# Optimization experiments

Measured on AMD Instinct MI355X. Metric: run time of the kernel, lower is better.

The kernel has to match this reference:

```python
import jax, jax.numpy as jnp
import numpy as np

RADIUS = 0.4
K = 32
EPS = 1e-5


def ball_query(xyz, new_xyz, radius, k):
    """xyz: (B,N,3), new_xyz: (B,M,3) -> idx (B,M,k) int32.
    Replicates CUDA ball_query: first k points within radius (in index order),
    padded with the first found index."""
    N = xyz.shape[1]
    # squared distances (B,M,N)
    d2 = jnp.sum((new_xyz[:, :, None, :] - xyz[:, None, :, :]) ** 2, axis=-1)
    within = d2 < radius * radius
    order = jnp.arange(N, dtype=jnp.int32)
    key = jnp.where(within, order[None, None, :], N)
    idx_sorted = jnp.argsort(key, axis=-1)[..., :k].astype(jnp.int32)  # (B,M,k)
    cnt = within.sum(axis=-1)  # (B,M)
    first = idx_sorted[..., :1]
    slot = jnp.arange(k)[None, None, :]
    return jnp.where(slot < cnt[..., None], idx_sorted, first)


def gather_bmk(x_bnc, idx):
    """x_bnc: (B,N,C), idx: (B,M,K) -> (B,M,K,C)"""
    return jnp.take_along_axis(x_bnc[:, None, :, :], idx[..., None], axis=2)


def conv_bn_relu(x, w, b, gamma, beta):
    """x: (B,Cin,M,K); w: (Cout,Cin). 1x1 Conv2d + BatchNorm2d (train stats) + ReLU."""
    x = jnp.einsum('bcmk,oc->bomk', x, w) + b[None, :, None, None]
    mu = x.mean(axis=(0, 2, 3), keepdims=True)
    var = x.var(axis=(0, 2, 3), keepdims=True)
    x = gamma[None, :, None, None] * (x - mu) * jax.lax.rsqrt(var + EPS) + beta[None, :, None, None]
    return jax.nn.relu(x)


def setup_inputs() -> dict:
    key = jax.random.key(0)
    ks = jax.random.split(key, 16)
    B, N, C, M = 4, 16384, 128, 1024
    mlp = [131, 128, 128, 256]
    inp = {
        'points_xyz': jax.random.normal(ks[0], (B, N, 3), dtype=jnp.float32),
        'features': jax.random.normal(ks[1], (B, C, N), dtype=jnp.float32),
        'indices': jax.random.randint(ks[2], (B, M), 0, N, dtype=jnp.int32),
    }
    for i in range(3):
        cin, cout = mlp[i], mlp[i + 1]
        inp[f'w{i+1}'] = jax.random.normal(ks[3 + 4 * i], (cout, cin), dtype=jnp.float32) / np.sqrt(cin)
        inp[f'b{i+1}'] = jnp.zeros((cout,), dtype=jnp.float32)
        inp[f'g{i+1}'] = jnp.ones((cout,), dtype=jnp.float32)
        inp[f'beta{i+1}'] = jnp.zeros((cout,), dtype=jnp.float32)
    return inp


def reference(points_xyz, features, indices,
              w1, b1, g1, beta1, w2, b2, g2, beta2, w3, b3, g3, beta3):
    # sample centers: new_xyz (B,M,3)
    new_xyz = jnp.take_along_axis(points_xyz, indices[..., None], axis=1)
    # ball query + group
    idx = ball_query(points_xyz, new_xyz, RADIUS, K)            # (B,M,K)
    grouped_xyz = gather_bmk(points_xyz, idx) - new_xyz[:, :, None, :]  # (B,M,K,3)
    grouped_feat = gather_bmk(features.transpose(0, 2, 1), idx)         # (B,M,K,C)
    x = jnp.concatenate([grouped_xyz, grouped_feat], axis=-1)           # (B,M,K,3+C)
    x = x.transpose(0, 3, 1, 2)                                         # (B,3+C,M,K)
    # shared MLP (1x1 Conv2d + BN + ReLU)
    x = conv_bn_relu(x, w1, b1, g1, beta1)
    x = conv_bn_relu(x, w2, b2, g2, beta2)
    x = conv_bn_relu(x, w3, b3, g3, beta3)
    # max pool over K -> (B, Cout, M)
    new_features = x.max(axis=-1)
    return new_xyz, new_features
```

## Files before the change

### kernel.cpp

```cpp
#include <hip/hip_runtime.h>

#define B_ 4
#define N_ 16384
#define C_ 128
#define M_ 1024
#define K_ 32
#define NTOT (B_*M_*K_)
#define RAD2 0.16f
#define EPS_ 1e-5f

typedef unsigned short ushort_t;
typedef __bf16 bf16x8 __attribute__((ext_vector_type(8)));
typedef float f32x4 __attribute__((ext_vector_type(4)));

__device__ __forceinline__ float b2f(ushort_t u){
  unsigned int x = ((unsigned int)u) << 16;
  return __builtin_bit_cast(float, x);
}
__device__ __forceinline__ ushort_t f2b(float f){
  return __builtin_bit_cast(ushort_t, (__bf16)f);
}

__global__ __launch_bounds__(256) void prep_all_k(
    const float* __restrict__ feat, ushort_t* __restrict__ ftr_t,
    const float* __restrict__ xyz, const int* __restrict__ indices,
    float* __restrict__ new_xyz, int* __restrict__ idx,
    const float* __restrict__ w1, const float* __restrict__ w2, const float* __restrict__ w3,
    ushort_t* __restrict__ W1b, ushort_t* __restrict__ W2b, ushort_t* __restrict__ W3b,
    float* __restrict__ stats)
{
  __shared__ float T[32][133];
  int bid = blockIdx.x;
  int t = threadIdx.x;

  if (bid < 1024){
    int wv = t >> 6, lane = t & 63;
    int g = bid*4 + wv;
    int b = g >> 10;
    const float* pb = xyz + (size_t)b*N_*3;
    const float4* pb4 = (const float4*)pb;
    int qi = indices[g];
    float qx = pb[qi*3+0], qy = pb[qi*3+1], qz = pb[qi*3+2];
    if (lane < 3) new_xyz[g*3 + lane] = pb[qi*3 + lane];

    int cnt = 0, firstIdx = 0;
    int* op = idx + g*K_;

    float4 buf0[6], buf1[6];
    #pragma unroll
    for (int i = 0; i < 6; i++) buf0[i] = pb4[lane*6 + i];

    unsigned long long below = (lane == 0) ? 0ull : ((~0ull) >> (64 - lane));

    auto process = [&](const float4* buf, int chunk){
      const float* f = (const float*)buf;
      unsigned int local_mask = 0;
      #pragma unroll
      for (int j = 0; j < 8; j++){
        float dx = f[j*3+0]-qx, dy = f[j*3+1]-qy, dz = f[j*3+2]-qz;
        if (dx*dx + dy*dy + dz*dz < RAD2) local_mask |= (1u << j);
      }
      unsigned long long many = __ballot(local_mask != 0);
      if (many == 0ull) return;
      int base = chunk*512;
      unsigned long long mj[8];
      #pragma unroll
      for (int j = 0; j < 8; j++) mj[j] = __ballot((local_mask >> j) & 1u);
      int excl = 0, total = 0;
      #pragma unroll
      for (int j = 0; j < 8; j++){
        excl  += __popcll(mj[j] & below);
        total += __popcll(mj[j]);
      }
      if (cnt == 0){
        int l0 = __builtin_ctzll(many);
        int j0 = 0;
        #pragma unroll
        for (int j = 7; j >= 0; j--) if ((mj[j] >> l0) & 1ull) j0 = j;
        firstIdx = base + l0*8 + j0;
      }
      int sl = cnt + excl;
      unsigned int m = local_mask;
      while (m && sl < K_){
        int j = __builtin_ctz(m); m &= m - 1u;
        op[sl++] = base + lane*8 + j;
      }
      cnt += total;
    };

    for (int chunk = 0; chunk < 32; chunk += 2){
      if (chunk + 1 < 32){
        #pragma unroll
        for (int i = 0; i < 6; i++) buf1[i] = pb4[(chunk+1)*384 + lane*6 + i];
      }
      process(buf0, chunk);
      if (cnt >= K_) break;
      if (chunk + 2 < 32){
        #pragma unroll
        for (int i = 0; i < 6; i++) buf0[i] = pb4[(chunk+2)*384 + lane*6 + i];
      }
      process(buf1, chunk + 1);
      if (cnt >= K_) break;
    }
    if (cnt < K_){
      for (int s = cnt + lane; s < K_; s += 64) op[s] = firstIdx;
    }
  } else if (bid < 3072){
    int bb = bid - 1024;
    int b = bb >> 9, ntile = bb & 511;
    int n0 = ntile * 32;
    int nl = t & 31;
    #pragma unroll
    for (int ci = 0; ci < 16; ci++){
      int c = ci*8 + (t >> 5);
      T[nl][c] = feat[((size_t)b*C_ + c)*N_ + n0 + nl];
    }
    __syncthreads();
    #pragma unroll
    for (int ii = 0; ii < 2; ii++){
      int v = ii*256 + t;
      int n2 = v >> 4, seg = v & 15;
      union { ushort_t u[8]; uint4 q; } pk;
      #pragma unroll
      for (int j = 0; j < 8; j++) pk.u[j] = f2b(T[n2][seg*8 + j]);
      *(uint4*)(ftr_t + ((size_t)b*N_ + n0 + n2)*C_ + seg*8) = pk.q;
    }
  } else {
    const int T1 = 128*160, T2 = 128*128;
    int e = (bid - 3072)*256 + t;
    if (e < T1){
      int o = e / 160, c = e % 160;
      float v = 0.f;
      if (c < 128) v = w1[o*131 + 3 + c];
      else if (c < 131) v = w1[o*131 + (c - 128)];
      W1b[e] = f2b(v);
    } else if (e < T1+T2){
      int e2 = e - T1;
      W2b[e2] = f2b(w2[e2]);
    } else {
      int e3 = e - T1 - T2;
      W3b[e3] = f2b(w3[e3]);
    }
    if (bid == 3072){
      #pragma unroll
      for (int j = 0; j < 6; j++) stats[j*256 + t] = 0.f;
    }
  }
}

__global__ __launch_bounds__(256, 4) void conv1_k(
    const float* __restrict__ xyz, const ushort_t* __restrict__ ftr_t,
    const int* __restrict__ idx, const float* __restrict__ new_xyz,
    const ushort_t* __restrict__ W1b, const float* __restrict__ b1,
    ushort_t* __restrict__ Y1, float* __restrict__ sumO, float* __restrict__ sqO)
{
  __shared__ alignas(16) ushort_t Xs[2][32*168];
  __shared__ alignas(16) float Ys[2][32*68];
  int t = threadIdx.x;
  int wv = t >> 6, lane = t & 63, quad = lane >> 4, l15 = lane & 15;
  int row = t >> 3, chunk = t & 7;
  int col0 = (blockIdx.x & 1) * 64;
  int blk = blockIdx.x >> 1;

  if (t < 128){
    int rr = t >> 2, cc = t & 3;
    *(uint4*)(Xs[0] + rr*168 + 128 + cc*8) = make_uint4(0,0,0,0);
    *(uint4*)(Xs[1] + rr*168 + 128 + cc*8) = make_uint4(0,0,0,0);
  }
  bf16x8 wf[5];
  #pragma unroll
  for (int kt = 0; kt < 5; kt++)
    wf[kt] = *(const bf16x8*)(W1b + (col0 + wv*16 + l15)*160 + kt*32 + quad*8);
  float bs_r = b1[col0 + wv*16 + l15];
  float s = 0.f, s2 = 0.f;

  const int GPB = 8;
  int g0 = blk * GPB;
  int b = g0 >> 10;
  int ia[GPB], ibv[GPB];
  #pragma unroll
  for (int i = 0; i < GPB; i++){
    ia[i]  = idx[(g0+i)*K_ + row];
    ibv[i] = idx[(g0+i)*K_ + (t & 31)];
  }
  uint4 r0, r1;
  float p3x, p3y, p3z, q3x, q3y, q3z;
  {
    const ushort_t* src = ftr_t + ((size_t)b*N_ + ia[0])*C_ + chunk*16;
    r0 = *(const uint4*)src; r1 = *(const uint4*)(src + 8);
    if (t < 32){
      const float* pp = xyz + ((size_t)b*N_ + ibv[0])*3;
      const float* qq = new_xyz + (size_t)g0*3;
      p3x = pp[0]; p3y = pp[1]; p3z = pp[2];
      q3x = qq[0]; q3y = qq[1]; q3z = qq[2];
    }
  }
  for (int i = 0; i < GPB; i++){
    int p = i & 1;
    ushort_t* X = Xs[p];
    *(uint4*)(X + row*168 + chunk*16) = r0;
    *(uint4*)(X + row*168 + chunk*16 + 8) = r1;
    if (t < 32){
      unsigned int u0 = (unsigned int)f2b(p3x-q3x) | ((unsigned int)f2b(p3y-q3y) << 16);
      unsigned int u1 = (unsigned int)f2b(p3z-q3z);
      *(uint2*)(X + t*168 + 128) = make_uint2(u0, u1);
    }
    if (i + 1 < GPB){
      const ushort_t* src = ftr_t + ((size_t)b*N_ + ia[i+1])*C_ + chunk*16;
      r0 = *(const uint4*)src; r1 = *(const uint4*)(src + 8);
      if (t < 32){
        const float* pp = xyz + ((size_t)b*N_ + ibv[i+1])*3;
        const float* qq = new_xyz + (size_t)(g0+i+1)*3;
        p3x = pp[0]; p3y = pp[1]; p3z = pp[2];
        q3x = qq[0]; q3y = qq[1]; q3z = qq[2];
      }
    }
    __syncthreads();
    bf16x8 af[2][5];
    #pragma unroll
    for (int mt = 0; mt < 2; mt++)
      #pragma unroll
      for (int kt = 0; kt < 5; kt++)
        af[mt][kt] = *(const bf16x8*)(X + (mt*16 + l15)*168 + kt*32 + quad*8);
    f32x4 acc[2] = {(f32x4){0,0,0,0}, (f32x4){0,0,0,0}};
    #pragma unroll
    for (int kt = 0; kt < 5; kt++){
      acc[0] = __builtin_amdgcn_mfma_f32_16x16x32_bf16(af[0][kt], wf[kt], acc[0], 0,0,0);
      acc[1] = __builtin_amdgcn_mfma_f32_16x16x32_bf16(af[1][kt], wf[kt], acc[1], 0,0,0);
    }
    {
      int o = wv*16 + l15;
      float* Yw = Ys[p];
      #pragma unroll
      for (int mt = 0; mt < 2; mt++)
        #pragma unroll
        for (int r = 0; r < 4; r++){
          float v = acc[mt][r] + bs_r;
          s += v; s2 += v*v;
          Yw[(mt*16 + quad*4 + r)*68 + o] = v;
        }
    }
    if (i > 0){
      const float* yp = &Ys[p^1][row*68 + chunk*8];
      f32x4 y0 = *(const f32x4*)(yp);
      f32x4 y1 = *(const f32x4*)(yp + 4);
      union { ushort_t u[8]; uint4 q; } p0;
      #pragma unroll
      for (int j = 0; j < 4; j++){
        p0.u[j] = f2b(y0[j]); p0.u[4+j] = f2b(y1[j]);
      }
      *(uint4*)(Y1 + ((size_t)(g0+i-1)*K_ + row)*128 + col0 + chunk*8) = p0.q;
    }
  }
  __syncthreads();
  {
    const float* yp = &Ys[(GPB-1)&1][row*68 + chunk*8];
    f32x4 y0 = *(const f32x4*)(yp);
    f32x4 y1 = *(const f32x4*)(yp + 4);
    union { ushort_t u[8]; uint4 q; } p0;
    #pragma unroll
    for (int j = 0; j < 4; j++){
      p0.u[j] = f2b(y0[j]); p0.u[4+j] = f2b(y1[j]);
    }
    *(uint4*)(Y1 + ((size_t)(g0+GPB-1)*K_ + row)*128 + col0 + chunk*8) = p0.q;
  }
  s  += __shfl_xor(s, 16);  s  += __shfl_xor(s, 32);
  s2 += __shfl_xor(s2, 16); s2 += __shfl_xor(s2, 32);
  if (quad == 0){
    int o = col0 + wv*16 + l15;
    atomicAdd(&sumO[o], s);
    atomicAdd(&sqO[o], s2);
  }
}

template<int COUT, bool MAXMIN, int MINB>
__global__ __launch_bounds__(256, MINB) void convB_k(
    const ushort_t* __restrict__ Yin, const ushort_t* __restrict__ Wb,
    const float* __restrict__ bias, const float* __restrict__ g_bn,
    const float* __restrict__ beta_bn, const float* __restrict__ sumI,
    const float* __restrict__ sqI, ushort_t* __restrict__ Yout,
    unsigned int* __restrict__ Ymm, float* __restrict__ sumO, float* __restrict__ sqO)
{
  constexpr int HALF = COUT/2;
  constexpr int NT = HALF/64;
  __shared__ alignas(16) ushort_t Xs[2][32*136];
  __shared__ alignas(16) float Ys[MAXMIN ? 1 : 2][MAXMIN ? 4 : 32*68];
  int t = threadIdx.x;
  int wv = t >> 6, lane = t & 63, quad = lane >> 4, l15 = lane & 15;
  int row = t >> 3, chunk = t & 7;
  int col0 = (blockIdx.x & 1) * HALF;
  int blk = blockIdx.x >> 1;

  float a_r[16], d_r[16];
  #pragma unroll
  for (int j = 0; j < 16; j++){
    int c = chunk*16 + j;
    float mu  = sumI[c] * (1.f/NTOT);
    float var = sqI[c]  * (1.f/NTOT) - mu*mu;
    float a = g_bn[c] * rsqrtf(var + EPS_);
    a_r[j] = a; d_r[j] = beta_bn[c] - a*mu;
  }
  bf16x8 wf[NT][4];
  #pragma unroll
  for (int nt = 0; nt < NT; nt++)
    #pragma unroll
    for (int kt = 0; kt < 4; kt++)
      wf[nt][kt] = *(const bf16x8*)(Wb + (col0 + wv*(NT*16) + nt*16 + l15)*128 + kt*32 + quad*8);
  float bs_r[NT];
  #pragma unroll
  for (int nt = 0; nt < NT; nt++) bs_r[nt] = bias[col0 + wv*(NT*16) + nt*16 + l15];
  float s[NT], s2[NT];
  #pragma unroll
  for (int nt = 0; nt < NT; nt++){ s[nt] = 0.f; s2[nt] = 0.f; }

  const int GPB = 8;
  int g0 = blk * GPB;
  uint4 r0, r1;
  {
    const ushort_t* src = Yin + ((size_t)g0*K_ + row)*128 + chunk*16;
    r0 = *(const uint4*)src; r1 = *(const uint4*)(src + 8);
  }
  for (int i = 0; i < GPB; i++){
    int p = i & 1;
    int g = g0 + i;
    ushort_t* X = Xs[p];
    union { ushort_t u[8]; uint4 q; } i0, i1, o0, o1;
    i0.q = r0; i1.q = r1;
    #pragma unroll
    for (int j = 0; j < 8; j++){
      o0.u[j] = f2b(fmaxf(a_r[j]  *b2f(i0.u[j]) + d_r[j],   0.f));
      o1.u[j] = f2b(fmaxf(a_r[8+j]*b2f(i1.u[j]) + d_r[8+j], 0.f));
    }
    *(uint4*)(X + row*136 + chunk*16) = o0.q;
    *(uint4*)(X + row*136 + chunk*16 + 8) = o1.q;
    if (i + 1 < GPB){
      const ushort_t* src = Yin + ((size_t)(g+1)*K_ + row)*128 + chunk*16;
      r0 = *(const uint4*)src; r1 = *(const uint4*)(src + 8);
    }
    __syncthreads();
    f32x4 acc[NT][2];
    #pragma unroll
    for (int nt = 0; nt < NT; nt++){ acc[nt][0] = (f32x4){0,0,0,0}; acc[nt][1] = (f32x4){0,0,0,0}; }
    #pragma unroll
    for (int kt = 0; kt < 4; kt++){
      bf16x8 A0 = *(const bf16x8*)(X + (l15)*136      + kt*32 + quad*8);
      bf16x8 A1 = *(const bf16x8*)(X + (16 + l15)*136 + kt*32 + quad*8);
      #pragma unroll
      for (int nt = 0; nt < NT; nt++){
        acc[nt][0] = __builtin_amdgcn_mfma_f32_16x16x32_bf16(A0, wf[nt][kt], acc[nt][0], 0,0,0);
        acc[nt][1] = __builtin_amdgcn_mfma_f32_16x16x32_bf16(A1, wf[nt][kt], acc[nt][1], 0,0,0);
      }
    }
    if constexpr (!MAXMIN){
      {
        int o = wv*16 + l15;
        float* Yw = Ys[p];
        #pragma unroll
        for (int mt = 0; mt < 2; mt++)
          #pragma unroll
          for (int r = 0; r < 4; r++){
            float v = acc[0][mt][r] + bs_r[0];
            s[0] += v; s2[0] += v*v;
            Yw[(mt*16 + quad*4 + r)*68 + o] = v;
          }
      }
      if (i > 0){
        const float* yp = &Ys[p^1][row*68 + chunk*8];
        f32x4 y0 = *(const f32x4*)(yp);
        f32x4 y1 = *(const f32x4*)(yp + 4);
        union { ushort_t u[8]; uint4 q; } p0;
        #pragma unroll
        for (int j = 0; j < 4; j++){
          p0.u[j] = f2b(y0[j]); p0.u[4+j] = f2b(y1[j]);
        }
        *(uint4*)(Yout + ((size_t)(g-1)*K_ + row)*128 + col0 + chunk*8) = p0.q;
      }
    } else {
      #pragma unroll
      for (int nt = 0; nt < NT; nt++){
        float v0 = acc[nt][0][0] + bs_r[nt];
        float mx = v0, mn = v0;
        s[nt] += v0; s2[nt] += v0*v0;
        #pragma unroll
        for (int mt = 0; mt < 2; mt++)
          #pragma unroll
          for (int r = 0; r < 4; r++){
            if (mt == 0 && r == 0) continue;
            float v = acc[nt][mt][r] + bs_r[nt];
            s[nt] += v; s2[nt] += v*v;
            mx = fmaxf(mx, v); mn = fminf(mn, v);
          }
        mx = fmaxf(mx, __shfl_xor(mx, 16)); mx = fmaxf(mx, __shfl_xor(mx, 32));
        mn = fminf(mn, __shfl_xor(mn, 16)); mn = fminf(mn, __shfl_xor(mn, 32));
        if (quad == 0){
          int o = col0 + wv*(NT*16) + nt*16 + l15;
          Ymm[(size_t)g*256 + o] = (unsigned int)f2b(mx) | ((unsigned int)f2b(mn) << 16);
        }
      }
    }
  }
  if constexpr (!MAXMIN){
    __syncthreads();
    const float* yp = &Ys[(GPB-1)&1][row*68 + chunk*8];
    f32x4 y0 = *(const f32x4*)(yp);
    f32x4 y1 = *(const f32x4*)(yp + 4);
    union { ushort_t u[8]; uint4 q; } p0;
    #pragma unroll
    for (int j = 0; j < 4; j++){
      p0.u[j] = f2b(y0[j]); p0.u[4+j] = f2b(y1[j]);
    }
    *(uint4*)(Yout + ((size_t)(g0+GPB-1)*K_ + row)*128 + col0 + chunk*8) = p0.q;
  }
  #pragma unroll
  for (int nt = 0; nt < NT; nt++){
    s[nt]  += __shfl_xor(s[nt], 16);  s[nt]  += __shfl_xor(s[nt], 32);
    s2[nt] += __shfl_xor(s2[nt], 16); s2[nt] += __shfl_xor(s2[nt], 32);
    if (quad == 0){
      int o = col0 + wv*(NT*16) + nt*16 + l15;
      atomicAdd(&sumO[o], s[nt]);
      atomicAdd(&sqO[o], s2[nt]);
    }
  }
}

__global__ __launch_bounds__(256) void finalize_k(
    const unsigned int* __restrict__ Ymm, const float* __restrict__ g3,
    const float* __restrict__ beta3, const float* __restrict__ sum3,
    const float* __restrict__ sq3, float* __restrict__ out)
{
  __shared__ float T[16][264];
  __shared__ float abn[256], dbn[256];
  int t = threadIdx.x;
  int b = blockIdx.x >> 6;
  int m0 = (blockIdx.x & 63) * 16;
  {
    float mu  = sum3[t] * (1.f/NTOT);
    float var = sq3[t]  * (1.f/NTOT) - mu*mu;
    float a = g3[t] * rsqrtf(var + EPS_);
    abn[t] = a; dbn[t] = beta3[t] - a*mu;
  }
  __syncthreads();
  #pragma unroll
  for (int i = 0; i < 4; i++){
    int v4 = i*256 + t;
    int m = v4 >> 6, oq = (v4 & 63) * 4;
    uint4 w = *(const uint4*)(Ymm + ((size_t)(b*M_ + m0 + m))*256 + oq);
    unsigned int wsv[4] = {w.x, w.y, w.z, w.w};
    float r[4];
    #pragma unroll
    for (int j = 0; j < 4; j++){
      int o = oq + j;
      float mx = b2f((ushort_t)(wsv[j] & 0xffffu));
      float mn = b2f((ushort_t)(wsv[j] >> 16));
      float a = abn[o];
      float val = (a >= 0.f) ? (a*mx + dbn[o]) : (a*mn + dbn[o]);
      r[j] = fmaxf(val, 0.f);
    }
    *(f32x4*)(&T[m][oq]) = *(f32x4*)r;
  }
  __syncthreads();
  #pragma unroll
  for (int p = 0; p < 4; p++){
    int o = p*64 + (t >> 2), c = t & 3;
    float4 v = make_float4(T[c*4+0][o], T[c*4+1][o], T[c*4+2][o], T[c*4+3][o]);
    *(float4*)(out + ((size_t)(b*256 + o))*M_ + m0 + c*4) = v;
  }
}

extern "C" void kernel_launch(void* const* d_in, const int* in_sizes, int n_in,
                              void* d_out, int out_size, void* d_ws, size_t ws_size,
                              hipStream_t stream)
{
  (void)in_sizes; (void)n_in; (void)out_size; (void)ws_size;
  const float* xyz  = (const float*)d_in[0];
  const float* feat = (const float*)d_in[1];
  const int*   inds = (const int*)d_in[2];
  const float* w1 = (const float*)d_in[3];
  const float* b1 = (const float*)d_in[4];
  const float* g1 = (const float*)d_in[5];
  const float* be1= (const float*)d_in[6];
  const float* w2 = (const float*)d_in[7];
  const float* b2 = (const float*)d_in[8];
  const float* g2 = (const float*)d_in[9];
  const float* be2= (const float*)d_in[10];
  const float* w3 = (const float*)d_in[11];
  const float* b3 = (const float*)d_in[12];
  const float* g3 = (const float*)d_in[13];
  const float* be3= (const float*)d_in[14];

  char* ws = (char*)d_ws;
  float* stats = (float*)ws;
  float* s1sum = stats + 0*256;  float* s1sq = stats + 1*256;
  float* s2sum = stats + 2*256;  float* s2sq = stats + 3*256;
  float* s3sum = stats + 4*256;  float* s3sq = stats + 5*256;
  size_t off = 6*256*sizeof(float);
  int* idx = (int*)(ws + off);                off += (size_t)B_*M_*K_*4;
  ushort_t* ftr_t = (ushort_t*)(ws + off);    off += (size_t)B_*N_*C_*2;
  ushort_t* W1b = (ushort_t*)(ws + off);      off += 128*160*2;
  ushort_t* W2b = (ushort_t*)(ws + off);      off += 128*128*2;
  ushort_t* W3b = (ushort_t*)(ws + off);      off += 256*128*2;
  ushort_t* Y1 = (ushort_t*)(ws + off);       off += (size_t)NTOT*128*2;
  ushort_t* Y2 = (ushort_t*)(ws + off);       off += (size_t)NTOT*128*2;
  unsigned int* Ymm = (unsigned int*)(ws + off); off += (size_t)B_*M_*256*4;

  float* new_xyz  = (float*)d_out;
  float* out_feat = (float*)d_out + (size_t)B_*M_*3;

  prep_all_k<<<3344, 256, 0, stream>>>(feat, ftr_t, xyz, inds, new_xyz, idx,
                                       w1, w2, w3, W1b, W2b, W3b, stats);
  conv1_k<<<1024, 256, 0, stream>>>(xyz, ftr_t, idx, new_xyz, W1b, b1, Y1, s1sum, s1sq);
  convB_k<128,false,4><<<1024, 256, 0, stream>>>(Y1, W2b, b2, g1, be1, s1sum, s1sq, Y2, nullptr, s2sum, s2sq);
  convB_k<256,true ,4><<<1024, 256, 0, stream>>>(Y2, W3b, b3, g2, be2, s2sum, s2sq, nullptr, Ymm, s3sum, s3sq);
  finalize_k<<<256, 256, 0, stream>>>(Ymm, g3, be3, s3sum, s3sq, out_feat);
}
```

Before: 209.4 us.

## Fuse ball query into conv1 kernel with pairwise inter-block spin barrier

Moves the ball-query work out of the prep kernel and into the first conv kernel. Each block computes the neighbour indices for 4 groups, then syncs with its partner block through a global atomic counter before both consume the 8 groups' indices. This shrinks the prep kernel and overlaps the ball query with conv1's per-block work, at the cost of a spin-wait that assumes both blocks in a pair are co-resident, which risks deadlock or stalls.

```diff
diff --git a/kernel.cpp b/kernel.cpp
--- a/kernel.cpp
+++ b/kernel.cpp
@@ -21,93 +21,18 @@
   return __builtin_bit_cast(ushort_t, (__bf16)f);
 }
 
-__global__ __launch_bounds__(256) void prep_all_k(
+__global__ __launch_bounds__(256) void prep2_k(
     const float* __restrict__ feat, ushort_t* __restrict__ ftr_t,
-    const float* __restrict__ xyz, const int* __restrict__ indices,
-    float* __restrict__ new_xyz, int* __restrict__ idx,
     const float* __restrict__ w1, const float* __restrict__ w2, const float* __restrict__ w3,
     ushort_t* __restrict__ W1b, ushort_t* __restrict__ W2b, ushort_t* __restrict__ W3b,
-    float* __restrict__ stats)
+    float* __restrict__ stats, unsigned int* __restrict__ pairbar)
 {
   __shared__ float T[32][133];
   int bid = blockIdx.x;
   int t = threadIdx.x;
 
-  if (bid < 1024){
-    int wv = t >> 6, lane = t & 63;
-    int g = bid*4 + wv;
-    int b = g >> 10;
-    const float* pb = xyz + (size_t)b*N_*3;
-    const float4* pb4 = (const float4*)pb;
-    int qi = indices[g];
-    float qx = pb[qi*3+0], qy = pb[qi*3+1], qz = pb[qi*3+2];
-    if (lane < 3) new_xyz[g*3 + lane] = pb[qi*3 + lane];
-
-    int cnt = 0, firstIdx = 0;
-    int* op = idx + g*K_;
-
-    float4 buf0[6], buf1[6];
-    #pragma unroll
-    for (int i = 0; i < 6; i++) buf0[i] = pb4[lane*6 + i];
-
-    unsigned long long below = (lane == 0) ? 0ull : ((~0ull) >> (64 - lane));
-
-    auto process = [&](const float4* buf, int chunk){
-      const float* f = (const float*)buf;
-      unsigned int local_mask = 0;
-      #pragma unroll
-      for (int j = 0; j < 8; j++){
-        float dx = f[j*3+0]-qx, dy = f[j*3+1]-qy, dz = f[j*3+2]-qz;
-        if (dx*dx + dy*dy + dz*dz < RAD2) local_mask |= (1u << j);
-      }
-      unsigned long long many = __ballot(local_mask != 0);
-      if (many == 0ull) return;
-      int base = chunk*512;
-      unsigned long long mj[8];
-      #pragma unroll
-      for (int j = 0; j < 8; j++) mj[j] = __ballot((local_mask >> j) & 1u);
-      int excl = 0, total = 0;
-      #pragma unroll
-      for (int j = 0; j < 8; j++){
-        excl  += __popcll(mj[j] & below);
-        total += __popcll(mj[j]);
-      }
-      if (cnt == 0){
-        int l0 = __builtin_ctzll(many);
-        int j0 = 0;
-        #pragma unroll
-        for (int j = 7; j >= 0; j--) if ((mj[j] >> l0) & 1ull) j0 = j;
-        firstIdx = base + l0*8 + j0;
-      }
-      int sl = cnt + excl;
-      unsigned int m = local_mask;
-      while (m && sl < K_){
-        int j = __builtin_ctz(m); m &= m - 1u;
-        op[sl++] = base + lane*8 + j;
-      }
-      cnt += total;
-    };
-
-    for (int chunk = 0; chunk < 32; chunk += 2){
-      if (chunk + 1 < 32){
-        #pragma unroll
-        for (int i = 0; i < 6; i++) buf1[i] = pb4[(chunk+1)*384 + lane*6 + i];
-      }
-      process(buf0, chunk);
-      if (cnt >= K_) break;
-      if (chunk + 2 < 32){
-        #pragma unroll
-        for (int i = 0; i < 6; i++) buf0[i] = pb4[(chunk+2)*384 + lane*6 + i];
-      }
-      process(buf1, chunk + 1);
-      if (cnt >= K_) break;
-    }
-    if (cnt < K_){
-      for (int s = cnt + lane; s < K_; s += 64) op[s] = firstIdx;
-    }
-  } else if (bid < 3072){
-    int bb = bid - 1024;
-    int b = bb >> 9, ntile = bb & 511;
+  if (bid < 2048){
+    int b = bid >> 9, ntile = bid & 511;
     int n0 = ntile * 32;
     int nl = t & 31;
     #pragma unroll
@@ -125,9 +50,9 @@
       for (int j = 0; j < 8; j++) pk.u[j] = f2b(T[n2][seg*8 + j]);
       *(uint4*)(ftr_t + ((size_t)b*N_ + n0 + n2)*C_ + seg*8) = pk.q;
     }
-  } else {
+  } else if (bid < 2320){
     const int T1 = 128*160, T2 = 128*128;
-    int e = (bid - 3072)*256 + t;
+    int e = (bid - 2048)*256 + t;
     if (e < T1){
       int o = e / 160, c = e % 160;
       float v = 0.f;
@@ -141,107 +66,209 @@
       int e3 = e - T1 - T2;
       W3b[e3] = f2b(w3[e3]);
     }
-    if (bid == 3072){
-      #pragma unroll
-      for (int j = 0; j < 6; j++) stats[j*256 + t] = 0.f;
-    }
-  }
-}
-
-__global__ __launch_bounds__(256, 4) void conv1_k(
-    const float* __restrict__ xyz, const ushort_t* __restrict__ ftr_t,
-    const int* __restrict__ idx, const float* __restrict__ new_xyz,
+  } else {
+    #pragma unroll
+    for (int j = 0; j < 6; j++) stats[j*256 + t] = 0.f;
+    #pragma unroll
+    for (int j = t; j < 512; j += 256) pairbar[j] = 0u;
+  }
+}
+
+__global__ __launch_bounds__(256, 4) void ballconv1_k(
+    const float* __restrict__ xyz, const int* __restrict__ indices,
+    float* new_xyz, int* idx,
+    const ushort_t* __restrict__ ftr_t,
     const ushort_t* __restrict__ W1b, const float* __restrict__ b1,
-    ushort_t* __restrict__ Y1, float* __restrict__ sumO, float* __restrict__ sqO)
+    ushort_t* __restrict__ Y1, float* __restrict__ sumO, float* __restrict__ sqO,
+    unsigned int* pairbar)
 {
   __shared__ alignas(16) ushort_t Xs[2][32*168];
   __shared__ alignas(16) float Ys[2][32*68];
   int t = threadIdx.x;
-  int wv = t >> 6, lane = t & 63, quad = lane >> 4, l15 = lane & 15;
-  int row = t >> 3, chunk = t & 7;
-  int col0 = (blockIdx.x & 1) * 64;
-  int blk = blockIdx.x >> 1;
-
-  if (t < 128){
-    int rr = t >> 2, cc = t & 3;
-    *(uint4*)(Xs[0] + rr*168 + 128 + cc*8) = make_uint4(0,0,0,0);
-    *(uint4*)(Xs[1] + rr*168 + 128 + cc*8) = make_uint4(0,0,0,0);
-  }
-  bf16x8 wf[5];
-  #pragma unroll
-  for (int kt = 0; kt < 5; kt++)
-    wf[kt] = *(const bf16x8*)(W1b + (col0 + wv*16 + l15)*160 + kt*32 + quad*8);
-  float bs_r = b1[col0 + wv*16 + l15];
-  float s = 0.f, s2 = 0.f;
-
-  const int GPB = 8;
-  int g0 = blk * GPB;
-  int b = g0 >> 10;
-  int ia[GPB], ibv[GPB];
-  #pragma unroll
-  for (int i = 0; i < GPB; i++){
-    ia[i]  = idx[(g0+i)*K_ + row];
-    ibv[i] = idx[(g0+i)*K_ + (t & 31)];
-  }
-  uint4 r0, r1;
-  float p3x, p3y, p3z, q3x, q3y, q3z;
+  int bid = blockIdx.x;
+
   {
-    const ushort_t* src = ftr_t + ((size_t)b*N_ + ia[0])*C_ + chunk*16;
-    r0 = *(const uint4*)src; r1 = *(const uint4*)(src + 8);
-    if (t < 32){
-      const float* pp = xyz + ((size_t)b*N_ + ibv[0])*3;
-      const float* qq = new_xyz + (size_t)g0*3;
-      p3x = pp[0]; p3y = pp[1]; p3z = pp[2];
-      q3x = qq[0]; q3y = qq[1]; q3z = qq[2];
-    }
-  }
-  for (int i = 0; i < GPB; i++){
-    int p = i & 1;
-    ushort_t* X = Xs[p];
-    *(uint4*)(X + row*168 + chunk*16) = r0;
-    *(uint4*)(X + row*168 + chunk*16 + 8) = r1;
-    if (t < 32){
-      unsigned int u0 = (unsigned int)f2b(p3x-q3x) | ((unsigned int)f2b(p3y-q3y) << 16);
-      unsigned int u1 = (unsigned int)f2b(p3z-q3z);
-      *(uint2*)(X + t*168 + 128) = make_uint2(u0, u1);
-    }
-    if (i + 1 < GPB){
-      const ushort_t* src = ftr_t + ((size_t)b*N_ + ia[i+1])*C_ + chunk*16;
+    int wv = t >> 6, lane = t & 63;
+    int g = bid*4 + wv;
+    int b = g >> 10;
+    const float* pb = xyz + (size_t)b*N_*3;
+    const float4* pb4 = (const float4*)pb;
+    int qi = indices[g];
+    float qx = pb[qi*3+0], qy = pb[qi*3+1], qz = pb[qi*3+2];
+    if (lane < 3) new_xyz[g*3 + lane] = pb[qi*3 + lane];
+
+    int cnt = 0, firstIdx = 0;
+    int* op = idx + g*K_;
+
+    float4 buf0[6], buf1[6];
+    #pragma unroll
+    for (int i = 0; i < 6; i++) buf0[i] = pb4[lane*6 + i];
+
+    unsigned long long below = (lane == 0) ? 0ull : ((~0ull) >> (64 - lane));
+
+    auto process = [&](const float4* buf, int chunk){
+      const float* f = (const float*)buf;
+      unsigned int local_mask = 0;
+      #pragma unroll
+      for (int j = 0; j < 8; j++){
+        float dx = f[j*3+0]-qx, dy = f[j*3+1]-qy, dz = f[j*3+2]-qz;
+        if (dx*dx + dy*dy + dz*dz < RAD2) local_mask |= (1u << j);
+      }
+      unsigned long long many = __ballot(local_mask != 0);
+      if (many == 0ull) return;
+      int base = chunk*512;
+      unsigned long long mj[8];
+      #pragma unroll
+      for (int j = 0; j < 8; j++) mj[j] = __ballot((local_mask >> j) & 1u);
+      int excl = 0, total = 0;
+      #pragma unroll
+      for (int j = 0; j < 8; j++){
+        excl  += __popcll(mj[j] & below);
+        total += __popcll(mj[j]);
+      }
+      if (cnt == 0){
+        int l0 = __builtin_ctzll(many);
+        int j0 = 0;
+        #pragma unroll
+        for (int j = 7; j >= 0; j--) if ((mj[j] >> l0) & 1ull) j0 = j;
+        firstIdx = base + l0*8 + j0;
+      }
+      int sl = cnt + excl;
+      unsigned int m = local_mask;
+      while (m && sl < K_){
+        int j = __builtin_ctz(m); m &= m - 1u;
+        op[sl++] = base + lane*8 + j;
+      }
+      cnt += total;
+    };
+
+    for (int chunk = 0; chunk < 32; chunk += 2){
+      if (chunk + 1 < 32){
+        #pragma unroll
+        for (int i = 0; i < 6; i++) buf1[i] = pb4[(chunk+1)*384 + lane*6 + i];
+      }
+      process(buf0, chunk);
+      if (cnt >= K_) break;
+      if (chunk + 2 < 32){
+        #pragma unroll
+        for (int i = 0; i < 6; i++) buf0[i] = pb4[(chunk+2)*384 + lane*6 + i];
+      }
+      process(buf1, chunk + 1);
+      if (cnt >= K_) break;
+    }
+    if (cnt < K_){
+      for (int s = cnt + lane; s < K_; s += 64) op[s] = firstIdx;
+    }
+  }
+
+  __syncthreads();
+  __threadfence();
+  if (t == 0){
+    __hip_atomic_fetch_add(&pairbar[bid >> 1], 1u, __ATOMIC_RELEASE, __HIP_MEMORY_SCOPE_AGENT);
+    while (__hip_atomic_load(&pairbar[bid >> 1], __ATOMIC_ACQUIRE, __HIP_MEMORY_SCOPE_AGENT) < 2u) {}
+  }
+  __syncthreads();
+  __threadfence();
+
+  {
+    int wv = t >> 6, lane = t & 63, quad = lane >> 4, l15 = lane & 15;
+    int row = t >> 3, chunk = t & 7;
+    int col0 = (bid & 1) * 64;
+    int blk = bid >> 1;
+
+    if (t < 128){
+      int rr = t >> 2, cc = t & 3;
+      *(uint4*)(Xs[0] + rr*168 + 128 + cc*8) = make_uint4(0,0,0,0);
+      *(uint4*)(Xs[1] + rr*168 + 128 + cc*8) = make_uint4(0,0,0,0);
+    }
+    bf16x8 wf[5];
+    #pragma unroll
+    for (int kt = 0; kt < 5; kt++)
+      wf[kt] = *(const bf16x8*)(W1b + (col0 + wv*16 + l15)*160 + kt*32 + quad*8);
+    float bs_r = b1[col0 + wv*16 + l15];
+    float s = 0.f, s2 = 0.f;
+
+    const int GPB = 8;
+    int g0 = blk * GPB;
+    int b = g0 >> 10;
+    int ia[GPB], ibv[GPB];
+    #pragma unroll
+    for (int i = 0; i < GPB; i++){
+      ia[i]  = idx[(g0+i)*K_ + row];
+      ibv[i] = idx[(g0+i)*K_ + (t & 31)];
+    }
+    uint4 r0, r1;
+    float p3x, p3y, p3z, q3x, q3y, q3z;
+    {
+      const ushort_t* src = ftr_t + ((size_t)b*N_ + ia[0])*C_ + chunk*16;
       r0 = *(const uint4*)src; r1 = *(const uint4*)(src + 8);
       if (t < 32){
-        const float* pp = xyz + ((size_t)b*N_ + ibv[i+1])*3;
-        const float* qq = new_xyz + (size_t)(g0+i+1)*3;
+        const float* pp = xyz + ((size_t)b*N_ + ibv[0])*3;
+        const float* qq = new_xyz + (size_t)g0*3;
         p3x = pp[0]; p3y = pp[1]; p3z = pp[2];
         q3x = qq[0]; q3y = qq[1]; q3z = qq[2];
       }
     }
+    for (int i = 0; i < GPB; i++){
+      int p = i & 1;
+      ushort_t* X = Xs[p];
+      *(uint4*)(X + row*168 + chunk*16) = r0;
+      *(uint4*)(X + row*168 + chunk*16 + 8) = r1;
+      if (t < 32){
+        unsigned int u0 = (unsigned int)f2b(p3x-q3x) | ((unsigned int)f2b(p3y-q3y) << 16);
+        unsigned int u1 = (unsigned int)f2b(p3z-q3z);
+        *(uint2*)(X + t*168 + 128) = make_uint2(u0, u1);
+      }
+      if (i + 1 < GPB){
+        const ushort_t* src = ftr_t + ((size_t)b*N_ + ia[i+1])*C_ + chunk*16;
+        r0 = *(const uint4*)src; r1 = *(const uint4*)(src + 8);
+        if (t < 32){
+          const float* pp = xyz + ((size_t)b*N_ + ibv[i+1])*3;
+          const float* qq = new_xyz + (size_t)(g0+i+1)*3;
+          p3x = pp[0]; p3y = pp[1]; p3z = pp[2];
+          q3x = qq[0]; q3y = qq[1]; q3z = qq[2];
+        }
+      }
+      __syncthreads();
+      bf16x8 af[2][5];
+      #pragma unroll
+      for (int mt = 0; mt < 2; mt++)
+        #pragma unroll
+        for (int kt = 0; kt < 5; kt++)
+          af[mt][kt] = *(const bf16x8*)(X + (mt*16 + l15)*168 + kt*32 + quad*8);
+      f32x4 acc[2] = {(f32x4){0,0,0,0}, (f32x4){0,0,0,0}};
+      #pragma unroll
+      for (int kt = 0; kt < 5; kt++){
+        acc[0] = __builtin_amdgcn_mfma_f32_16x16x32_bf16(af[0][kt], wf[kt], acc[0], 0,0,0);
+        acc[1] = __builtin_amdgcn_mfma_f32_16x16x32_bf16(af[1][kt], wf[kt], acc[1], 0,0,0);
+      }
+      {
+        int o = wv*16 + l15;
+        float* Yw = Ys[p];
+        #pragma unroll
+        for (int mt = 0; mt < 2; mt++)
+          #pragma unroll
+          for (int r = 0; r < 4; r++){
+            float v = acc[mt][r] + bs_r;
+            s += v; s2 += v*v;
+            Yw[(mt*16 + quad*4 + r)*68 + o] = v;
+          }
+      }
+      if (i > 0){
+        const float* yp = &Ys[p^1][row*68 + chunk*8];
+        f32x4 y0 = *(const f32x4*)(yp);
+        f32x4 y1 = *(const f32x4*)(yp + 4);
+        union { ushort_t u[8]; uint4 q; } p0;
+        #pragma unroll
+        for (int j = 0; j < 4; j++){
+          p0.u[j] = f2b(y0[j]); p0.u[4+j] = f2b(y1[j]);
+        }
+        *(uint4*)(Y1 + ((size_t)(g0+i-1)*K_ + row)*128 + col0 + chunk*8) = p0.q;
+      }
+    }
     __syncthreads();
-    bf16x8 af[2][5];
-    #pragma unroll
-    for (int mt = 0; mt < 2; mt++)
-      #pragma unroll
-      for (int kt = 0; kt < 5; kt++)
-        af[mt][kt] = *(const bf16x8*)(X + (mt*16 + l15)*168 + kt*32 + quad*8);
-    f32x4 acc[2] = {(f32x4){0,0,0,0}, (f32x4){0,0,0,0}};
-    #pragma unroll
-    for (int kt = 0; kt < 5; kt++){
-      acc[0] = __builtin_amdgcn_mfma_f32_16x16x32_bf16(af[0][kt], wf[kt], acc[0], 0,0,0);
-      acc[1] = __builtin_amdgcn_mfma_f32_16x16x32_bf16(af[1][kt], wf[kt], acc[1], 0,0,0);
-    }
     {
-      int o = wv*16 + l15;
-      float* Yw = Ys[p];
-      #pragma unroll
-      for (int mt = 0; mt < 2; mt++)
-        #pragma unroll
-        for (int r = 0; r < 4; r++){
-          float v = acc[mt][r] + bs_r;
-          s += v; s2 += v*v;
-          Yw[(mt*16 + quad*4 + r)*68 + o] = v;
-        }
-    }
-    if (i > 0){
-      const float* yp = &Ys[p^1][row*68 + chunk*8];
+      const float* yp = &Ys[(GPB-1)&1][row*68 + chunk*8];
       f32x4 y0 = *(const f32x4*)(yp);
       f32x4 y1 = *(const f32x4*)(yp + 4);
       union { ushort_t u[8]; uint4 q; } p0;
@@ -249,27 +276,15 @@
       for (int j = 0; j < 4; j++){
         p0.u[j] = f2b(y0[j]); p0.u[4+j] = f2b(y1[j]);
       }
-      *(uint4*)(Y1 + ((size_t)(g0+i-1)*K_ + row)*128 + col0 + chunk*8) = p0.q;
-    }
-  }
-  __syncthreads();
-  {
-    const float* yp = &Ys[(GPB-1)&1][row*68 + chunk*8];
-    f32x4 y0 = *(const f32x4*)(yp);
-    f32x4 y1 = *(const f32x4*)(yp + 4);
-    union { ushort_t u[8]; uint4 q; } p0;
-    #pragma unroll
-    for (int j = 0; j < 4; j++){
-      p0.u[j] = f2b(y0[j]); p0.u[4+j] = f2b(y1[j]);
-    }
-    *(uint4*)(Y1 + ((size_t)(g0+GPB-1)*K_ + row)*128 + col0 + chunk*8) = p0.q;
-  }
-  s  += __shfl_xor(s, 16);  s  += __shfl_xor(s, 32);
-  s2 += __shfl_xor(s2, 16); s2 += __shfl_xor(s2, 32);
-  if (quad == 0){
-    int o = col0 + wv*16 + l15;
-    atomicAdd(&sumO[o], s);
-    atomicAdd(&sqO[o], s2);
+      *(uint4*)(Y1 + ((size_t)(g0+GPB-1)*K_ + row)*128 + col0 + chunk*8) = p0.q;
+    }
+    s  += __shfl_xor(s, 16);  s  += __shfl_xor(s, 32);
+    s2 += __shfl_xor(s2, 16); s2 += __shfl_xor(s2, 32);
+    if (quad == 0){
+      int o = col0 + wv*16 + l15;
+      atomicAdd(&sumO[o], s);
+      atomicAdd(&sqO[o], s2);
+    }
   }
 }
 
@@ -494,6 +509,7 @@
   float* s2sum = stats + 2*256;  float* s2sq = stats + 3*256;
   float* s3sum = stats + 4*256;  float* s3sq = stats + 5*256;
   size_t off = 6*256*sizeof(float);
+  unsigned int* pairbar = (unsigned int*)(ws + off); off += 512*sizeof(unsigned int);
   int* idx = (int*)(ws + off);                off += (size_t)B_*M_*K_*4;
   ushort_t* ftr_t = (ushort_t*)(ws + off);    off += (size_t)B_*N_*C_*2;
   ushort_t* W1b = (ushort_t*)(ws + off);      off += 128*160*2;
@@ -506,9 +522,10 @@
   float* new_xyz  = (float*)d_out;
   float* out_feat = (float*)d_out + (size_t)B_*M_*3;
 
-  prep_all_k<<<3344, 256, 0, stream>>>(feat, ftr_t, xyz, inds, new_xyz, idx,
-                                       w1, w2, w3, W1b, W2b, W3b, stats);
-  conv1_k<<<1024, 256, 0, stream>>>(xyz, ftr_t, idx, new_xyz, W1b, b1, Y1, s1sum, s1sq);
+  prep2_k<<<2321, 256, 0, stream>>>(feat, ftr_t, w1, w2, w3, W1b, W2b, W3b,
+                                    stats, pairbar);
+  ballconv1_k<<<1024, 256, 0, stream>>>(xyz, inds, new_xyz, idx, ftr_t,
+                                        W1b, b1, Y1, s1sum, s1sq, pairbar);
   convB_k<128,false,4><<<1024, 256, 0, stream>>>(Y1, W2b, b2, g1, be1, s1sum, s1sq, Y2, nullptr, s2sum, s2sq);
   convB_k<256,true ,4><<<1024, 256, 0, stream>>>(Y2, W3b, b3, g2, be2, s2sum, s2sq, nullptr, Ymm, s3sum, s3sq);
   finalize_k<<<256, 256, 0, stream>>>(Ymm, g3, be3, s3sum, s3sq, out_feat);
```

After: 483.5 us. 2.31x slower.
